# Kernel optimization log

Measured on AMD Instinct MI355X. Metric: run time of the kernel, lower is better.

## Reference

```python
import jax, jax.numpy as jnp
import numpy as np

B, S, D, E = 4, 4096, 1024, 8

def setup_inputs() -> dict:
    key = jax.random.key(0)
    k_h, k_wr, k_br, k_we = jax.random.split(key, 4)
    h = jax.random.normal(k_h, (B, S, D), dtype=jnp.float32)
    # route_weights: nn.Linear(D, E) -> weight [E, D], bias [E]
    W_route = jax.random.normal(k_wr, (E, D), dtype=jnp.float32) / np.sqrt(D)
    b_route = jax.random.normal(k_br, (E,), dtype=jnp.float32) * 0.01
    # edge_transforms: E x nn.Linear(D, D, bias=False) -> stacked [E, D_out, D_in]
    W_edges = jax.random.normal(k_we, (E, D, D), dtype=jnp.float32) / np.sqrt(D)
    layer_bias = jnp.zeros((D,), dtype=jnp.float32)
    return {"h": h, "W_route": W_route, "b_route": b_route,
            "W_edges": W_edges, "layer_bias": layer_bias}

def reference(h, W_route, b_route, W_edges, layer_bias):
    # route_logits = h @ W_route.T + b_route -> [B, S, E]
    route_logits = jnp.einsum('bsd,ed->bse', h, W_route) + b_route
    rw = jax.nn.softmax(route_logits, axis=-1)
    # fused: sum_e rw[b,s,e] * (h @ W_e.T) -> [B, S, D]
    out = jnp.einsum('bsd,efd,bse->bsf', h, W_edges, rw)
    out = out + layer_bias
    return jax.nn.gelu(out, approximate=False)  # torch F.gelu default is exact erf
```

## Files before the change

kernel.cpp:

```cpp
#include <hip/hip_runtime.h>
#include <hip/hip_bf16.h>

#define M_TOK 16384
#define DDIM  1024
#define NEXP  8
#define KP    (NEXP * DDIM)

typedef __bf16 bf16x8 __attribute__((ext_vector_type(8)));
typedef float  floatx4 __attribute__((ext_vector_type(4)));

__device__ __forceinline__ void gload_lds16(const void* g, void* l) {
    __builtin_amdgcn_global_load_lds(
        (__attribute__((address_space(1))) void*)(void*)g,
        (__attribute__((address_space(3))) void*)l,
        16, 0, 0);
}

__global__ __launch_bounds__(256) void route_kernel(
    const float* __restrict__ h, const float* __restrict__ Wr,
    const float* __restrict__ br, __bf16* __restrict__ hbf,
    float* __restrict__ rw)
{
    __shared__ float Wrs[NEXP * DDIM];
    const int tid = threadIdx.x;
    {
        const float4* s4 = (const float4*)Wr;
        float4* d4 = (float4*)Wrs;
        #pragma unroll
        for (int j = 0; j < 8; ++j) d4[j * 256 + tid] = s4[j * 256 + tid];
    }
    __syncthreads();

    const int wave = tid >> 6, lane = tid & 63;
    const int m = blockIdx.x * 4 + wave;

    const float4* hrow = (const float4*)(h + (size_t)m * DDIM + lane * 16);
    float a[16];
    #pragma unroll
    for (int i = 0; i < 4; ++i) {
        float4 v = hrow[i];
        a[i*4+0] = v.x; a[i*4+1] = v.y; a[i*4+2] = v.z; a[i*4+3] = v.w;
    }
    bf16x8 o0, o1;
    #pragma unroll
    for (int i = 0; i < 8; ++i) { o0[i] = (__bf16)a[i]; o1[i] = (__bf16)a[8 + i]; }
    *(bf16x8*)(hbf + (size_t)m * DDIM + lane * 16)     = o0;
    *(bf16x8*)(hbf + (size_t)m * DDIM + lane * 16 + 8) = o1;

    float p[NEXP];
    #pragma unroll
    for (int e = 0; e < NEXP; ++e) {
        const float4* w4 = (const float4*)&Wrs[e * DDIM + lane * 16];
        float s = 0.f;
        #pragma unroll
        for (int i = 0; i < 4; ++i) {
            float4 wv = w4[i];
            s += a[i*4+0]*wv.x + a[i*4+1]*wv.y + a[i*4+2]*wv.z + a[i*4+3]*wv.w;
        }
        p[e] = s;
    }
    #pragma unroll
    for (int e = 0; e < NEXP; ++e) {
        #pragma unroll
        for (int off = 32; off > 0; off >>= 1)
            p[e] += __shfl_xor(p[e], off, 64);
    }
    if (lane == 0) {
        float l[NEXP], mx = -1e30f;
        #pragma unroll
        for (int e = 0; e < NEXP; ++e) { l[e] = p[e] + br[e]; mx = fmaxf(mx, l[e]); }
        float s = 0.f;
        #pragma unroll
        for (int e = 0; e < NEXP; ++e) { l[e] = expf(l[e] - mx); s += l[e]; }
        float inv = 1.f / s;
        float4 r0 = {l[0]*inv, l[1]*inv, l[2]*inv, l[3]*inv};
        float4 r1 = {l[4]*inv, l[5]*inv, l[6]*inv, l[7]*inv};
        *(float4*)(rw + (size_t)m * NEXP)     = r0;
        *(float4*)(rw + (size_t)m * NEXP + 4) = r1;
    }
}

__global__ __launch_bounds__(256) void convw2_kernel(
    const float* __restrict__ src, __bf16* __restrict__ dst)
{
    size_t idx = ((size_t)blockIdx.x * 256 + threadIdx.x) * 16;
    int e = (int)(idx >> 20);
    int f = (int)(idx >> 10) & 1023;
    int k = (int)idx & 1023;
    const float4* s4 = (const float4*)(src + idx);
    float a[16];
    #pragma unroll
    for (int i = 0; i < 4; ++i) {
        float4 v = s4[i];
        a[i*4+0] = v.x; a[i*4+1] = v.y; a[i*4+2] = v.z; a[i*4+3] = v.w;
    }
    bf16x8 o0, o1;
    #pragma unroll
    for (int i = 0; i < 8; ++i) { o0[i] = (__bf16)a[i]; o1[i] = (__bf16)a[8 + i]; }
    __bf16* d = dst + (size_t)f * KP + (size_t)e * DDIM + k;
    *(bf16x8*)d       = o0;
    *(bf16x8*)(d + 8) = o1;
}

__global__ __launch_bounds__(256, 3) void gemm_fused_kernel(
    const __bf16* __restrict__ hbf, const __bf16* __restrict__ Bp,
    const float* __restrict__ rw, const float* __restrict__ bias,
    float* __restrict__ outp)
{
    __shared__ __bf16 As[128 * 64];
    __shared__ __bf16 Bs[128 * 64];
    __shared__ float  rws[128 * NEXP];

    const int tid  = threadIdx.x;
    const int wave = tid >> 6, lane = tid & 63;
    const int quad = lane >> 4, l16 = lane & 15;
    const int wm = wave & 1, wn = wave >> 1;
    const int m0 = blockIdx.y * 128, f0 = blockIdx.x * 128;

    {
        const float4* src = (const float4*)(rw + (size_t)m0 * NEXP);
        ((float4*)rws)[tid] = src[tid];
    }

    const floatx4 z4 = {0.f, 0.f, 0.f, 0.f};
    floatx4 facc[4][4];
    #pragma unroll
    for (int i = 0; i < 4; ++i) {
        #pragma unroll
        for (int j = 0; j < 4; ++j) facc[i][j] = z4;
    }

    int aslot[2][4], bslot[2][4];
    #pragma unroll
    for (int s = 0; s < 2; ++s) {
        #pragma unroll
        for (int f = 0; f < 4; ++f) {
            int ra = wm*64 + f*16 + l16;
            int rb = wn*64 + f*16 + l16;
            int grp = s*4 + quad;
            aslot[s][f] = ra*8 + ((grp ^ ra) & 7);
            bslot[s][f] = rb*8 + ((grp ^ rb) & 7);
        }
    }

    __syncthreads();

    float wcur[4][4];

    for (int e = 0; e < NEXP; ++e) {
        #pragma unroll
        for (int mf = 0; mf < 4; ++mf) {
            #pragma unroll
            for (int r = 0; r < 4; ++r) {
                float wn_ = fmaxf(rws[(wm*64 + mf*16 + quad*4 + r) * NEXP + e], 1e-20f);
                if (e > 0) {
                    float ratio = wcur[mf][r] / wn_;
                    #pragma unroll
                    for (int nf = 0; nf < 4; ++nf)
                        facc[mf][nf][r] *= ratio;
                }
                wcur[mf][r] = wn_;
            }
        }

        for (int k0 = 0; k0 < DDIM; k0 += 64) {
            __syncthreads();
            #pragma unroll
            for (int t = 0; t < 4; ++t) {
                int g   = t * 256 + tid;
                int row = g >> 3;
                int c   = ((g ^ row) & 7) * 8;
                gload_lds16(hbf + (size_t)(m0 + row) * DDIM + k0 + c,
                            (char*)As + g * 16);
                gload_lds16(Bp + (size_t)(f0 + row) * KP + e * DDIM + k0 + c,
                            (char*)Bs + g * 16);
            }
            __syncthreads();

            #pragma unroll
            for (int s = 0; s < 2; ++s) {
                bf16x8 av[4], bv[4];
                #pragma unroll
                for (int mf = 0; mf < 4; ++mf)
                    av[mf] = *(const bf16x8*)&As[aslot[s][mf] * 8];
                #pragma unroll
                for (int nf = 0; nf < 4; ++nf)
                    bv[nf] = *(const bf16x8*)&Bs[bslot[s][nf] * 8];
                #pragma unroll
                for (int mf = 0; mf < 4; ++mf) {
                    #pragma unroll
                    for (int nf = 0; nf < 4; ++nf)
                        facc[mf][nf] = __builtin_amdgcn_mfma_f32_16x16x32_bf16(
                            av[mf], bv[nf], facc[mf][nf], 0, 0, 0);
                }
            }
        }
    }

    #pragma unroll
    for (int nf = 0; nf < 4; ++nf) {
        int gf = f0 + wn*64 + nf*16 + l16;
        float bval = bias[gf];
        #pragma unroll
        for (int mf = 0; mf < 4; ++mf) {
            int gm = m0 + wm*64 + mf*16 + quad*4;
            #pragma unroll
            for (int r = 0; r < 4; ++r) {
                float x = facc[mf][nf][r] * wcur[mf][r] + bval;
                float gel = 0.5f * x * (1.0f + erff(x * 0.70710678118f));
                outp[(size_t)(gm + r) * DDIM + gf] = gel;
            }
        }
    }
}

extern "C" void kernel_launch(void* const* d_in, const int* in_sizes, int n_in,
                              void* d_out, int out_size, void* d_ws, size_t ws_size,
                              hipStream_t stream) {
    const float* h    = (const float*)d_in[0];
    const float* Wr   = (const float*)d_in[1];
    const float* br   = (const float*)d_in[2];
    const float* We   = (const float*)d_in[3];
    const float* bias = (const float*)d_in[4];
    float* outp = (float*)d_out;
    char* ws = (char*)d_ws;

    __bf16* hbf = (__bf16*)ws;
    __bf16* Bp  = (__bf16*)(ws + (size_t)M_TOK * DDIM * 2);
    float*  rwp = (float*)(ws + (size_t)M_TOK * DDIM * 2
                              + (size_t)NEXP * DDIM * DDIM * 2);

    hipLaunchKernelGGL(route_kernel, dim3(M_TOK / 4), dim3(256), 0, stream,
                       h, Wr, br, hbf, rwp);
    hipLaunchKernelGGL(convw2_kernel, dim3((NEXP * DDIM * DDIM) / (256 * 16)),
                       dim3(256), 0, stream, We, Bp);
    hipLaunchKernelGGL(gemm_fused_kernel, dim3(DDIM / 128, M_TOK / 128),
                       dim3(256), 0, stream, hbf, Bp, rwp, bias, outp);
}
```

Measured before the change: 506.9 us.

## Switch GEMM to 32x32x16 MFMA and precompute routing weight ratios in route kernel

Replaces the 16x16x32 bf16 MFMA tiles with 32x32x16 tiles, giving fewer, larger matrix instructions and fewer LDS fragment loads per k-step. The route kernel now writes successive weight ratios w[e]/w[e+1] plus the final weight, so the GEMM rescales accumulators with a multiply instead of a per-element division. It also drops the LDS staging of the routing weights in the route kernel and reads them directly from global memory. The accumulator layout and epilogue indexing change to match the 32x32 output fragment layout, which risks indexing mistakes.

```diff
diff --git a/kernel.cpp b/kernel.cpp
--- a/kernel.cpp
+++ b/kernel.cpp
@@ -6,8 +6,9 @@
 #define NEXP  8
 #define KP    (NEXP * DDIM)
 
-typedef __bf16 bf16x8 __attribute__((ext_vector_type(8)));
+typedef __bf16 bf16x8  __attribute__((ext_vector_type(8)));
 typedef float  floatx4 __attribute__((ext_vector_type(4)));
+typedef float  floatx16 __attribute__((ext_vector_type(16)));
 
 __device__ __forceinline__ void gload_lds16(const void* g, void* l) {
     __builtin_amdgcn_global_load_lds(
@@ -21,16 +22,7 @@
     const float* __restrict__ br, __bf16* __restrict__ hbf,
     float* __restrict__ rw)
 {
-    __shared__ float Wrs[NEXP * DDIM];
     const int tid = threadIdx.x;
-    {
-        const float4* s4 = (const float4*)Wr;
-        float4* d4 = (float4*)Wrs;
-        #pragma unroll
-        for (int j = 0; j < 8; ++j) d4[j * 256 + tid] = s4[j * 256 + tid];
-    }
-    __syncthreads();
-
     const int wave = tid >> 6, lane = tid & 63;
     const int m = blockIdx.x * 4 + wave;
 
@@ -50,7 +42,7 @@
     float p[NEXP];
     #pragma unroll
     for (int e = 0; e < NEXP; ++e) {
-        const float4* w4 = (const float4*)&Wrs[e * DDIM + lane * 16];
+        const float4* w4 = (const float4*)(Wr + e * DDIM + lane * 16);
         float s = 0.f;
         #pragma unroll
         for (int i = 0; i < 4; ++i) {
@@ -73,8 +65,15 @@
         #pragma unroll
         for (int e = 0; e < NEXP; ++e) { l[e] = expf(l[e] - mx); s += l[e]; }
         float inv = 1.f / s;
-        float4 r0 = {l[0]*inv, l[1]*inv, l[2]*inv, l[3]*inv};
-        float4 r1 = {l[4]*inv, l[5]*inv, l[6]*inv, l[7]*inv};
+        float w[NEXP];
+        #pragma unroll
+        for (int e = 0; e < NEXP; ++e) w[e] = fmaxf(l[e] * inv, 1e-20f);
+        float o[NEXP];
+        #pragma unroll
+        for (int e = 0; e < NEXP - 1; ++e) o[e] = w[e] / w[e + 1];
+        o[7] = w[7];
+        float4 r0 = {o[0], o[1], o[2], o[3]};
+        float4 r1 = {o[4], o[5], o[6], o[7]};
         *(float4*)(rw + (size_t)m * NEXP)     = r0;
         *(float4*)(rw + (size_t)m * NEXP + 4) = r1;
     }
@@ -113,7 +112,7 @@
 
     const int tid  = threadIdx.x;
     const int wave = tid >> 6, lane = tid & 63;
-    const int quad = lane >> 4, l16 = lane & 15;
+    const int half = lane >> 5, l32 = lane & 31;
     const int wm = wave & 1, wn = wave >> 1;
     const int m0 = blockIdx.y * 128, f0 = blockIdx.x * 128;
 
@@ -122,44 +121,40 @@
         ((float4*)rws)[tid] = src[tid];
     }
 
-    const floatx4 z4 = {0.f, 0.f, 0.f, 0.f};
-    floatx4 facc[4][4];
-    #pragma unroll
-    for (int i = 0; i < 4; ++i) {
-        #pragma unroll
-        for (int j = 0; j < 4; ++j) facc[i][j] = z4;
-    }
-
-    int aslot[2][4], bslot[2][4];
-    #pragma unroll
-    for (int s = 0; s < 2; ++s) {
-        #pragma unroll
-        for (int f = 0; f < 4; ++f) {
-            int ra = wm*64 + f*16 + l16;
-            int rb = wn*64 + f*16 + l16;
-            int grp = s*4 + quad;
-            aslot[s][f] = ra*8 + ((grp ^ ra) & 7);
-            bslot[s][f] = rb*8 + ((grp ^ rb) & 7);
+    floatx16 facc[2][2];
+    #pragma unroll
+    for (int i = 0; i < 2; ++i)
+        #pragma unroll
+        for (int j = 0; j < 2; ++j)
+            #pragma unroll
+            for (int r = 0; r < 16; ++r) facc[i][j][r] = 0.f;
+
+    int aslot[4][2], bslot[4][2];
+    #pragma unroll
+    for (int ks = 0; ks < 4; ++ks) {
+        #pragma unroll
+        for (int b = 0; b < 2; ++b) {
+            int ra = wm*64 + b*32 + l32;
+            int rb = wn*64 + b*32 + l32;
+            int grp = ks*2 + half;
+            aslot[ks][b] = ra*8 + ((grp ^ ra) & 7);
+            bslot[ks][b] = rb*8 + ((grp ^ rb) & 7);
         }
     }
 
     __syncthreads();
 
-    float wcur[4][4];
-
     for (int e = 0; e < NEXP; ++e) {
-        #pragma unroll
-        for (int mf = 0; mf < 4; ++mf) {
-            #pragma unroll
-            for (int r = 0; r < 4; ++r) {
-                float wn_ = fmaxf(rws[(wm*64 + mf*16 + quad*4 + r) * NEXP + e], 1e-20f);
-                if (e > 0) {
-                    float ratio = wcur[mf][r] / wn_;
-                    #pragma unroll
-                    for (int nf = 0; nf < 4; ++nf)
-                        facc[mf][nf][r] *= ratio;
+        if (e > 0) {
+            #pragma unroll
+            for (int mb = 0; mb < 2; ++mb) {
+                #pragma unroll
+                for (int r = 0; r < 16; ++r) {
+                    int lrow = wm*64 + mb*32 + (r & 3) + 8*(r >> 2) + 4*half;
+                    float ratio = rws[lrow * NEXP + (e - 1)];
+                    facc[mb][0][r] *= ratio;
+                    facc[mb][1][r] *= ratio;
                 }
-                wcur[mf][r] = wn_;
             }
         }
 
@@ -178,37 +173,42 @@
             __syncthreads();
 
             #pragma unroll
-            for (int s = 0; s < 2; ++s) {
-                bf16x8 av[4], bv[4];
-                #pragma unroll
-                for (int mf = 0; mf < 4; ++mf)
-                    av[mf] = *(const bf16x8*)&As[aslot[s][mf] * 8];
-                #pragma unroll
-                for (int nf = 0; nf < 4; ++nf)
-                    bv[nf] = *(const bf16x8*)&Bs[bslot[s][nf] * 8];
-                #pragma unroll
-                for (int mf = 0; mf < 4; ++mf) {
+            for (int ks = 0; ks < 4; ++ks) {
+                bf16x8 av[2], bv[2];
+                #pragma unroll
+                for (int mb = 0; mb < 2; ++mb)
+                    av[mb] = *(const bf16x8*)&As[aslot[ks][mb] * 8];
+                #pragma unroll
+                for (int nb = 0; nb < 2; ++nb)
+                    bv[nb] = *(const bf16x8*)&Bs[bslot[ks][nb] * 8];
+                #pragma unroll
+                for (int mb = 0; mb < 2; ++mb) {
                     #pragma unroll
-                    for (int nf = 0; nf < 4; ++nf)
-                        facc[mf][nf] = __builtin_amdgcn_mfma_f32_16x16x32_bf16(
-                            av[mf], bv[nf], facc[mf][nf], 0, 0, 0);
+                    for (int nb = 0; nb < 2; ++nb)
+                        facc[mb][nb] = __builtin_amdgcn_mfma_f32_32x32x16_bf16(
+                            av[mb], bv[nb], facc[mb][nb], 0, 0, 0);
                 }
             }
         }
     }
 
-    #pragma unroll
-    for (int nf = 0; nf < 4; ++nf) {
-        int gf = f0 + wn*64 + nf*16 + l16;
-        float bval = bias[gf];
-        #pragma unroll
-        for (int mf = 0; mf < 4; ++mf) {
-            int gm = m0 + wm*64 + mf*16 + quad*4;
-            #pragma unroll
-            for (int r = 0; r < 4; ++r) {
-                float x = facc[mf][nf][r] * wcur[mf][r] + bval;
+    int col[2]; float bval[2];
+    #pragma unroll
+    for (int nb = 0; nb < 2; ++nb) {
+        col[nb] = f0 + wn*64 + nb*32 + l32;
+        bval[nb] = bias[col[nb]];
+    }
+    #pragma unroll
+    for (int mb = 0; mb < 2; ++mb) {
+        #pragma unroll
+        for (int r = 0; r < 16; ++r) {
+            int lrow = wm*64 + mb*32 + (r & 3) + 8*(r >> 2) + 4*half;
+            float w7 = rws[lrow * NEXP + 7];
+            #pragma unroll
+            for (int nb = 0; nb < 2; ++nb) {
+                float x = facc[mb][nb][r] * w7 + bval[nb];
                 float gel = 0.5f * x * (1.0f + erff(x * 0.70710678118f));
-                outp[(size_t)(gm + r) * DDIM + gf] = gel;
+                outp[(size_t)(m0 + lrow) * DDIM + col[nb]] = gel;
             }
         }
     }
```

Result: slower. 528.9 us (+4.3%).
